# Performance work log

Measured on AMD Instinct MI355X. Metric: run time of the kernel, lower is better.

The kernel has to match this reference:

```python
import jax, jax.numpy as jnp
import numpy as np

B, NE, NMAX = 256, 90, 270
ZE = PE = GE = PPS = 32
NPROPS = 20
FP, SGE, LATH = 256, 64, 128
PIN = FP + SGE + LATH  # 448 = pred_inp_size = conv input (add_to_node)
C1, C2, H = 448, 256, 3
P1 = P2 = 512
EPS = 1e-5

PNAMES = ['sg_emb_table','lat_W1','lat_b1','lat_bn1_g','lat_bn1_b','lat_bn1_m','lat_bn1_v',
          'lat_W2','lat_b2','lat_bn2_g','lat_bn2_b','lat_bn2_m','lat_bn2_v',
          'z_emb_table','period_table','group_table','props','W_props','b_props','W_phys','b_phys',
          'gat1_W','gat1_as','gat1_ad','gat1_b','gat2_W','gat2_as','gat2_ad','gat2_b',
          'pW1','pb1','pbn1_g','pbn1_b','pbn1_m','pbn1_v',
          'pW2','pb2','pbn2_g','pbn2_b','pbn2_m','pbn2_v','pW3','pb3']

def _bn(x, g, b, m, v):
    return (x - m) * g / jnp.sqrt(v + EPS) + b

def _lrelu(x, s=0.2):
    return jnp.where(x >= 0, x, s * x)

def _gat(x, adj, W, a_s, a_d, bias):
    # PyG DenseGATConv: concat=False (mean over heads), dropout=0, negative_slope=0.2
    Bn, N, _ = x.shape
    h = (x @ W).reshape(Bn, N, H, -1)                      # [B,N,H,C]
    asrc = (h * a_s).sum(-1)                               # [B,N,H]
    adst = (h * a_d).sum(-1)
    alpha = asrc[:, None, :, :] + adst[:, :, None, :]      # [B,i,j,H]
    alpha = _lrelu(alpha, 0.2)
    adj_sl = jnp.maximum(adj, jnp.eye(N, dtype=adj.dtype))  # add self loops
    alpha = jnp.where(adj_sl[..., None] > 0, alpha, -jnp.inf)
    alpha = jax.nn.softmax(alpha, axis=2)                  # softmax over sources j
    out = jnp.einsum('bijh,bjhc->bihc', alpha, h)
    return out.mean(2) + bias                              # [B,N,C]

def _forward(comp, sg, lat, period_idx, group_idx, p):
    sg_x = p['sg_emb_table'][sg[:, 0]]                     # [B,SGE]
    # lattice MLP: (Linear -> BN -> LeakyReLU(True)==identity) x2
    h = _bn(lat @ p['lat_W1'] + p['lat_b1'], p['lat_bn1_g'], p['lat_bn1_b'], p['lat_bn1_m'], p['lat_bn1_v'])
    lat_x = _bn(h @ p['lat_W2'] + p['lat_b2'], p['lat_bn2_g'], p['lat_bn2_b'], p['lat_bn2_m'], p['lat_bn2_v'])
    # ragged -> dense batch: expand composition counts into dense node-type grid
    n_atoms = comp.sum(1)                                  # [B]
    cum = jnp.cumsum(comp, axis=1)                         # [B,NE]
    t = jnp.arange(NMAX)
    z = jax.vmap(lambda c: jnp.searchsorted(c, t, side='right'))(cum)  # [B,NMAX]
    mask = t[None, :] < n_atoms[:, None]                   # [B,NMAX] valid nodes
    z = jnp.where(mask, z, 0)
    # PhysEmbedding: z/period/group embeddings + projected properties -> final proj
    phys = jnp.concatenate([
        p['z_emb_table'][z],
        p['period_table'][period_idx[z]],
        p['group_table'][group_idx[z]],
        p['props'][z] @ p['W_props'] + p['b_props'],
    ], axis=-1)
    phys = phys @ p['W_phys'] + p['b_phys']                # [B,NMAX,FP]
    # add_to_node: cat graph-level lat/sg embeddings onto every node, then zero-pad
    node = jnp.concatenate([
        phys,
        jnp.broadcast_to(lat_x[:, None, :], (lat_x.shape[0], NMAX, LATH)),
        jnp.broadcast_to(sg_x[:, None, :], (sg_x.shape[0], NMAX, SGE)),
    ], axis=-1)
    node = node * mask[..., None].astype(node.dtype)       # to_dense_batch zero padding
    # per-graph dense block adjacency, zero diagonal (fill_diagonal_(0))
    adj = (mask[:, :, None] & mask[:, None, :]).astype(node.dtype)
    adj = adj * (1.0 - jnp.eye(NMAX, dtype=node.dtype))
    # GNNBlock: act = LeakyReLU(True) == identity (negative_slope=1)
    x1 = _gat(node, adj, p['gat1_W'], p['gat1_as'], p['gat1_ad'], p['gat1_b'])
    x2 = _gat(x1, adj, p['gat2_W'], p['gat2_as'], p['gat2_ad'], p['gat2_b'])
    comp_x = x2.sum(1)                                     # sum over ALL NMAX slots (incl. padding, as torch does)
    feat = jnp.concatenate([comp_x, sg_x, lat_x], axis=-1) # [B,PIN]
    # prediction head (eval: dropout off, BN running stats)
    h = _lrelu(_bn(feat @ p['pW1'] + p['pb1'], p['pbn1_g'], p['pbn1_b'], p['pbn1_m'], p['pbn1_v']))
    h = _lrelu(_bn(h @ p['pW2'] + p['pb2'], p['pbn2_g'], p['pbn2_b'], p['pbn2_m'], p['pbn2_v']))
    return h @ p['pW3'] + p['pb3']                         # [B,1]

def setup_inputs():
    key = jax.random.key(0)
    ks = iter(jax.random.split(key, 64))
    def nrm(shape, s=0.05):
        return jax.random.normal(next(ks), shape, dtype=jnp.float32) * s
    comp = jax.random.randint(next(ks), (B, NE), 0, 4, dtype=jnp.int32)
    comp = comp.at[0].set(3)  # graph 0 has exactly NMAX atoms -> data N_max == NMAX
    sg = jax.random.randint(next(ks), (B, 1), 0, 230)
    lat = jax.random.uniform(next(ks), (B, 6), dtype=jnp.float32)
    period_idx = jax.random.randint(next(ks), (NE,), 0, 8)
    group_idx = jax.random.randint(next(ks), (NE,), 0, 19)
    inp = dict(comp=comp, sg=sg, lat=lat, period_idx=period_idx, group_idx=group_idx)
    inp.update(
        sg_emb_table=nrm((230, SGE)),
        lat_W1=nrm((6, LATH)), lat_b1=nrm((LATH,)),
        lat_bn1_g=jnp.ones(LATH), lat_bn1_b=jnp.zeros(LATH), lat_bn1_m=jnp.zeros(LATH), lat_bn1_v=jnp.ones(LATH),
        lat_W2=nrm((LATH, LATH)), lat_b2=nrm((LATH,)),
        lat_bn2_g=jnp.ones(LATH), lat_bn2_b=jnp.zeros(LATH), lat_bn2_m=jnp.zeros(LATH), lat_bn2_v=jnp.ones(LATH),
        z_emb_table=nrm((NE, ZE)), period_table=nrm((8, PE)), group_table=nrm((19, GE)),
        props=nrm((NE, NPROPS), 0.1), W_props=nrm((NPROPS, PPS)), b_props=nrm((PPS,)),
        W_phys=nrm((ZE + PE + GE + PPS, FP)), b_phys=nrm((FP,)),
        gat1_W=nrm((PIN, H * C1)), gat1_as=nrm((H, C1)), gat1_ad=nrm((H, C1)), gat1_b=nrm((C1,)),
        gat2_W=nrm((C1, H * C2)), gat2_as=nrm((H, C2)), gat2_ad=nrm((H, C2)), gat2_b=nrm((C2,)),
        pW1=nrm((PIN, P1)), pb1=nrm((P1,)),
        pbn1_g=jnp.ones(P1), pbn1_b=jnp.zeros(P1), pbn1_m=jnp.zeros(P1), pbn1_v=jnp.ones(P1),
        pW2=nrm((P1, P2)), pb2=nrm((P2,)),
        pbn2_g=jnp.ones(P2), pbn2_b=jnp.zeros(P2), pbn2_m=jnp.zeros(P2), pbn2_v=jnp.ones(P2),
        pW3=nrm((P2, 1)), pb3=nrm((1,)),
    )
    return inp

def reference(comp, sg, lat, period_idx, group_idx,
              sg_emb_table, lat_W1, lat_b1, lat_bn1_g, lat_bn1_b, lat_bn1_m, lat_bn1_v,
              lat_W2, lat_b2, lat_bn2_g, lat_bn2_b, lat_bn2_m, lat_bn2_v,
              z_emb_table, period_table, group_table, props, W_props, b_props, W_phys, b_phys,
              gat1_W, gat1_as, gat1_ad, gat1_b, gat2_W, gat2_as, gat2_ad, gat2_b,
              pW1, pb1, pbn1_g, pbn1_b, pbn1_m, pbn1_v,
              pW2, pb2, pbn2_g, pbn2_b, pbn2_m, pbn2_v, pW3, pb3):
    vals = (sg_emb_table, lat_W1, lat_b1, lat_bn1_g, lat_bn1_b, lat_bn1_m, lat_bn1_v,
            lat_W2, lat_b2, lat_bn2_g, lat_bn2_b, lat_bn2_m, lat_bn2_v,
            z_emb_table, period_table, group_table, props, W_props, b_props, W_phys, b_phys,
            gat1_W, gat1_as, gat1_ad, gat1_b, gat2_W, gat2_as, gat2_ad, gat2_b,
            pW1, pb1, pbn1_g, pbn1_b, pbn1_m, pbn1_v,
            pW2, pb2, pbn2_g, pbn2_b, pbn2_m, pbn2_v, pW3, pb3)
    p = dict(zip(PNAMES, vals))
    return _forward(comp, sg, lat, period_idx, group_idx, p)
```

## Files before the change

### kernel.cpp

```cpp
#include <hip/hip_runtime.h>
#include <math.h>

#define BB 256
#define NEL 90
#define NMAX 270
#define C1 448
#define C2 256
#define PIN 448
#define LATH 128
#define SGE 64
#define P1 512
#define EPSB 1e-5f

typedef short shortx8 __attribute__((ext_vector_type(8)));
typedef float floatx4 __attribute__((ext_vector_type(4)));

__device__ __forceinline__ float bf2f(unsigned short u) {
  return __uint_as_float(((unsigned)u) << 16);
}
__device__ __forceinline__ unsigned short f2bf(float f) {
  unsigned x = __float_as_uint(f);
  unsigned r = (x + 0x7fffu + ((x >> 16) & 1u)) >> 16;
  return (unsigned short)r;
}
__device__ __forceinline__ void gld16(const void* g, void* l) {
  __builtin_amdgcn_global_load_lds(
      (const __attribute__((address_space(1))) unsigned int*)g,
      (__attribute__((address_space(3))) unsigned int*)l, 16, 0, 0);
}

#define NB_PREP  BB
#define NB_SCAN  1
#define NB_PHYS  NEL
#define NB_WP1   (14 * 42)
#define NB_WP2   (14 * 24)
#define NB_FOLD  112
#define NB_PAD   64
#define SETUP_GRID (NB_PREP + NB_SCAN + NB_PHYS + NB_WP1 + NB_WP2 + 2 * NB_FOLD + NB_PAD)

__global__ __launch_bounds__(256) void k_setup(
    const int* __restrict__ comp, const int* __restrict__ sg, const float* __restrict__ lat,
    const float* __restrict__ sg_emb,
    const float* __restrict__ lW1, const float* __restrict__ lb1,
    const float* __restrict__ lg1, const float* __restrict__ lbe1,
    const float* __restrict__ lm1, const float* __restrict__ lv1,
    const float* __restrict__ lW2, const float* __restrict__ lb2,
    const float* __restrict__ lg2, const float* __restrict__ lbe2,
    const float* __restrict__ lm2, const float* __restrict__ lv2,
    const int* __restrict__ period_idx, const int* __restrict__ group_idx,
    const float* __restrict__ z_emb, const float* __restrict__ period_t,
    const float* __restrict__ group_t, const float* __restrict__ props,
    const float* __restrict__ Wp, const float* __restrict__ bp,
    const float* __restrict__ Wphys, const float* __restrict__ bphys,
    const float* __restrict__ gat1_W, const float* __restrict__ gat1_as,
    const float* __restrict__ gat1_ad, const float* __restrict__ gat1_b,
    const float* __restrict__ gat2_W, const float* __restrict__ gat2_as,
    const float* __restrict__ gat2_ad, const float* __restrict__ gat2_b,
    float* __restrict__ sgx, float* __restrict__ latx, int* __restrict__ z,
    int* __restrict__ natoms, int* __restrict__ off, int* __restrict__ aoff,
    float* __restrict__ zerobuf, float* __restrict__ physpe,
    unsigned short* __restrict__ wt1, unsigned short* __restrict__ wt2,
    float* __restrict__ wsv1, float* __restrict__ wdv1,
    float* __restrict__ wsv2, float* __restrict__ wdv2, float* __restrict__ pad2) {
  int r = blockIdx.x;
  int tid = threadIdx.x;
  int wv = tid >> 6, lane = tid & 63;

  if (r < NB_PREP) {
    int b = r;
    __shared__ int cum[NEL];
    __shared__ float hbuf[LATH];
    __shared__ float latl[6];
    if (tid == 0) {
      int s = 0;
      for (int e = 0; e < NEL; ++e) { s += comp[b * NEL + e]; cum[e] = s; }
    }
    if (tid < 6) latl[tid] = lat[b * 6 + tid];
    __syncthreads();
    int n = cum[NEL - 1];
    for (int t = tid; t < NMAX; t += 256) {
      int zz = -1;
      if (t < n) {
        for (int e = 0; e < NEL; ++e) { if (cum[e] > t) { zz = e; break; } }
      }
      z[b * NMAX + t] = zz;
    }
    if (tid < SGE) sgx[b * SGE + tid] = sg_emb[sg[b] * SGE + tid];
    if (tid < LATH) {
      float acc = lb1[tid];
      for (int k = 0; k < 6; ++k) acc += latl[k] * lW1[k * LATH + tid];
      acc = (acc - lm1[tid]) * lg1[tid] * rsqrtf(lv1[tid] + EPSB) + lbe1[tid];
      hbuf[tid] = acc;
    }
    __syncthreads();
    if (tid < LATH) {
      float acc = lb2[tid];
      for (int k = 0; k < LATH; ++k) acc += hbuf[k] * lW2[k * LATH + tid];
      acc = (acc - lm2[tid]) * lg2[tid] * rsqrtf(lv2[tid] + EPSB) + lbe2[tid];
      latx[b * LATH + tid] = acc;
    }
    return;
  }
  r -= NB_PREP;
  if (r < NB_SCAN) {
    __shared__ int sh[BB];
    zerobuf[tid] = 0.f;
    int v0 = 0;
    for (int e = 0; e < NEL; ++e) v0 += comp[tid * NEL + e];
    natoms[tid] = v0;
    sh[tid] = v0;
    for (int d = 1; d < BB; d <<= 1) {
      __syncthreads();
      int v = (tid >= d) ? sh[tid - d] : 0;
      __syncthreads();
      sh[tid] += v;
    }
    __syncthreads();
    off[tid] = sh[tid] - v0;
    __syncthreads();
    int sz = 3 * ((((v0 + 15) >> 4) << 4)) * ((((v0 + 31) >> 5) << 5));
    sh[tid] = sz;
    for (int d = 1; d < BB; d <<= 1) {
      __syncthreads();
      int v = (tid >= d) ? sh[tid - d] : 0;
      __syncthreads();
      sh[tid] += v;
    }
    __syncthreads();
    aoff[tid] = sh[tid] - sz;
    return;
  }
  r -= NB_SCAN;
  if (r < NB_PHYS) {
    int e = r;
    __shared__ float ph[128];
    if (tid < 32) ph[tid] = z_emb[e * 32 + tid];
    else if (tid < 64) ph[tid] = period_t[period_idx[e] * 32 + tid - 32];
    else if (tid < 96) ph[tid] = group_t[group_idx[e] * 32 + tid - 64];
    else if (tid < 128) {
      int j = tid - 96;
      float acc = bp[j];
      for (int k = 0; k < 20; ++k) acc += props[e * 20 + k] * Wp[k * 32 + j];
      ph[tid] = acc;
    }
    __syncthreads();
    float acc = bphys[tid];
    for (int k = 0; k < 128; ++k) acc += ph[k] * Wphys[k * 256 + tid];
    physpe[e * 256 + tid] = acc;
    return;
  }
  r -= NB_PHYS;
  if (r < NB_WP1 + NB_WP2) {
    const float* W;
    unsigned short* Wt;
    int NC3, bx, by;
    if (r < NB_WP1) { W = gat1_W; Wt = wt1; NC3 = 3 * C1; bx = r % 14; by = r / 14; }
    else { int r2 = r - NB_WP1; W = gat2_W; Wt = wt2; NC3 = 3 * C2; bx = r2 % 14; by = r2 / 14; }
    int k0 = bx << 5, c0 = by << 5;
    __shared__ float ts[32][33];
    int e4 = tid << 2;
    int kk = e4 >> 5, cc = e4 & 31;
    float4 v = *(const float4*)(W + (size_t)(k0 + kk) * NC3 + c0 + cc);
    ts[kk][cc] = v.x; ts[kk][cc + 1] = v.y; ts[kk][cc + 2] = v.z; ts[kk][cc + 3] = v.w;
    __syncthreads();
    int c2 = tid & 31, kg = tid >> 5;
    ushort4 u;
    u.x = f2bf(ts[kg * 4 + 0][c2]); u.y = f2bf(ts[kg * 4 + 1][c2]);
    u.z = f2bf(ts[kg * 4 + 2][c2]); u.w = f2bf(ts[kg * 4 + 3][c2]);
    *(ushort4*)(Wt + (size_t)(c0 + c2) * 448 + k0 + (kg << 2)) = u;
    return;
  }
  r -= NB_WP1 + NB_WP2;
  if (r < 2 * NB_FOLD) {
    const float* W; const float* as_; const float* ad_;
    float* wsv; float* wdv; int NC3, C, kb;
    if (r < NB_FOLD) { W = gat1_W; as_ = gat1_as; ad_ = gat1_ad; wsv = wsv1; wdv = wdv1; NC3 = 3 * C1; C = C1; kb = r << 2; }
    else { int r2 = r - NB_FOLD; W = gat2_W; as_ = gat2_as; ad_ = gat2_ad; wsv = wsv2; wdv = wdv2; NC3 = 3 * C2; C = C2; kb = r2 << 2; }
    int k = kb + wv;
    for (int h = 0; h < 3; ++h) {
      float ss = 0.f, sd = 0.f;
      for (int c = lane; c < C; c += 64) {
        float wvv = W[(size_t)k * NC3 + h * C + c];
        ss += wvv * as_[h * C + c];
        sd += wvv * ad_[h * C + c];
      }
      for (int o = 32; o > 0; o >>= 1) { ss += __shfl_xor(ss, o); sd += __shfl_xor(sd, o); }
      if (lane == 0) { wsv[k * 3 + h] = ss; wdv[k * 3 + h] = sd; }
    }
    return;
  }
  r -= 2 * NB_FOLD;
  {
    int c = (r << 2) + wv;
    float s = 0.f;
    for (int k = lane; k < C1; k += 64) {
      const float* wr = gat2_W + (size_t)k * (3 * C2) + c;
      s += gat1_b[k] * (wr[0] + wr[C2] + wr[2 * C2]);
    }
    for (int o = 32; o > 0; o >>= 1) s += __shfl_xor(s, o);
    if (lane == 0) pad2[c] = s * (1.f / 3.f) + gat2_b[c];
  }
}

__global__ __launch_bounds__(256) void k_nodep(
    const int* __restrict__ z, const int* __restrict__ off, const int* __restrict__ natoms,
    const float* __restrict__ physpe, const float* __restrict__ latx,
    const float* __restrict__ sgx, unsigned short* __restrict__ x0) {
  int b = blockIdx.x;
  int n = natoms[b], ob = off[b];
  int tid = threadIdx.x;
  __shared__ int zl[NMAX];
  for (int t = tid; t < n; t += 256) zl[t] = z[b * NMAX + t];
  __syncthreads();
  int items = n * 56;
  for (int e = tid; e < items; e += 256) {
    int t = e / 56, c8 = (e - t * 56) << 3;
    int zt = zl[t];
    float v[8];
    if (c8 < 256) {
      float4 a = *(const float4*)(physpe + zt * 256 + c8);
      float4 c = *(const float4*)(physpe + zt * 256 + c8 + 4);
      v[0] = a.x; v[1] = a.y; v[2] = a.z; v[3] = a.w;
      v[4] = c.x; v[5] = c.y; v[6] = c.z; v[7] = c.w;
    } else if (c8 < 384) {
      float4 a = *(const float4*)(latx + b * LATH + c8 - 256);
      float4 c = *(const float4*)(latx + b * LATH + c8 - 252);
      v[0] = a.x; v[1] = a.y; v[2] = a.z; v[3] = a.w;
      v[4] = c.x; v[5] = c.y; v[6] = c.z; v[7] = c.w;
    } else {
      float4 a = *(const float4*)(sgx + b * SGE + c8 - 384);
      float4 c = *(const float4*)(sgx + b * SGE + c8 - 380);
      v[0] = a.x; v[1] = a.y; v[2] = a.z; v[3] = a.w;
      v[4] = c.x; v[5] = c.y; v[6] = c.z; v[7] = c.w;
    }
    unsigned short u[8];
    #pragma unroll
    for (int i = 0; i < 8; ++i) u[i] = f2bf(v[i]);
    *(uint4*)(x0 + (size_t)(ob + t) * PIN + c8) = *(uint4*)u;
  }
}

__global__ __launch_bounds__(256) void k_av2(
    const unsigned short* __restrict__ x, const float* __restrict__ wsv,
    const float* __restrict__ wdv, const int* __restrict__ off,
    const int* __restrict__ natoms, float* __restrict__ asrc,
    float* __restrict__ adst, int K) {
  __shared__ float sw[C1 * 3], dw[C1 * 3];
  int tid = threadIdx.x;
  for (int e = tid; e < K * 3; e += 256) { sw[e] = wsv[e]; dw[e] = wdv[e]; }
  __syncthreads();
  int total = off[BB - 1] + natoms[BB - 1];
  int wv = tid >> 6, lane = tid & 63;
  int nk8 = K >> 3;
  int stride = gridDim.x << 2;
  for (int row = (blockIdx.x << 2) + wv; row < total; row += stride) {
    float s0 = 0.f, s1 = 0.f, s2 = 0.f, d0 = 0.f, d1 = 0.f, d2 = 0.f;
    if (lane < nk8) {
      uint4 raw = *(const uint4*)(x + (size_t)row * K + (lane << 3));
      unsigned short us[8];
      *(uint4*)us = raw;
      #pragma unroll
      for (int u = 0; u < 8; ++u) {
        float xv = bf2f(us[u]);
        int kb = ((lane << 3) + u) * 3;
        s0 += xv * sw[kb + 0]; s1 += xv * sw[kb + 1]; s2 += xv * sw[kb + 2];
        d0 += xv * dw[kb + 0]; d1 += xv * dw[kb + 1]; d2 += xv * dw[kb + 2];
      }
    }
    #pragma unroll
    for (int o = 32; o > 0; o >>= 1) {
      s0 += __shfl_xor(s0, o); s1 += __shfl_xor(s1, o); s2 += __shfl_xor(s2, o);
      d0 += __shfl_xor(d0, o); d1 += __shfl_xor(d1, o); d2 += __shfl_xor(d2, o);
    }
    if (lane == 0) {
      asrc[row * 3 + 0] = s0; asrc[row * 3 + 1] = s1; asrc[row * 3 + 2] = s2;
      adst[row * 3 + 0] = d0; adst[row * 3 + 1] = d1; adst[row * 3 + 2] = d2;
    }
  }
}

#define MTMAX 17
__global__ __launch_bounds__(256) void k_alpha(
    const float* __restrict__ asrc, const float* __restrict__ adst,
    const int* __restrict__ off, const int* __restrict__ natoms,
    const int* __restrict__ aoff, unsigned short* __restrict__ alpha) {
  int bid = blockIdx.x;
  int b = bid & (BB - 1);
  int hm = bid >> 8;
  int h = hm % 3;
  int mt = hm / 3;
  int n = natoms[b];
  if (n == 0) return;
  int mtn = (n + 15) >> 4;
  if (mt >= mtn) return;
  int ktn = (n + 31) >> 5;
  int rext = mtn << 4, kext = ktn << 5;
  int ob = off[b];
  size_t ab = (size_t)aoff[b] + (size_t)h * rext * kext;
  int tid = threadIdx.x;
  int wv = tid >> 6, lane = tid & 63;
  __shared__ float asl[288];
  for (int j = tid; j < kext; j += 256)
    asl[j] = (j < n) ? asrc[(ob + j) * 3 + h] : 0.f;
  __syncthreads();
  #pragma unroll
  for (int r = 0; r < 4; ++r) {
    int i = (mt << 4) + (wv << 2) + r;
    unsigned short* rowp = alpha + ab + (size_t)i * kext;
    if (i >= n) {
      for (int j = lane; j < kext; j += 64) rowp[j] = 0;
      continue;
    }
    float ad = adst[(ob + i) * 3 + h];
    float m = -1e30f;
    for (int j = lane; j < n; j += 64) {
      float sc = asl[j] + ad;
      sc = fmaxf(sc, 0.2f * sc);
      m = fmaxf(m, sc);
    }
    for (int o = 32; o > 0; o >>= 1) m = fmaxf(m, __shfl_xor(m, o));
    float s = 0.f;
    for (int j = lane; j < n; j += 64) {
      float sc = asl[j] + ad;
      sc = fmaxf(sc, 0.2f * sc);
      s += __expf(sc - m);
    }
    for (int o = 32; o > 0; o >>= 1) s += __shfl_xor(s, o);
    float rs = 1.f / s;
    for (int j = lane; j < kext; j += 64) {
      float v = 0.f;
      if (j < n) {
        float sc = asl[j] + ad;
        sc = fmaxf(sc, 0.2f * sc);
        v = __expf(sc - m) * rs;
      }
      rowp[j] = f2bf(v);
    }
  }
}

#define MTW 5

__global__ __launch_bounds__(256, 2) void k_fused_mfma(
    const unsigned short* __restrict__ xin, const unsigned short* __restrict__ Wt,
    const unsigned short* __restrict__ alpha, const int* __restrict__ aoff,
    const int* __restrict__ off, const int* __restrict__ natoms,
    const float* __restrict__ bias, const float* __restrict__ zerobuf,
    unsigned short* __restrict__ xout, int K, int C, int NC) {
  int bid = blockIdx.x;
  int xg = bid & 7;
  int g = bid >> 3;
  int cblk = g % NC;
  int b = xg + ((g / NC) << 3);
  int c0 = cblk << 6;
  int n = natoms[b];
  if (n == 0) return;
  int ob = off[b];
  size_t ab = (size_t)aoff[b];
  int tid = threadIdx.x;
  int wv = tid >> 6;
  int lane = tid & 63;
  int m16 = lane & 15;
  int q = lane >> 4;

  int mtn = (n + 15) >> 4;
  int jmax = mtn << 4;
  int ktn = (n + 31) >> 5;
  int kext = ktn << 5;
  size_t hstride = (size_t)jmax * kext;

  __shared__ unsigned short xs0[17 * 512];
  __shared__ unsigned short tt[36 * 512];

  const unsigned short* xsrc[MTW];
  #pragma unroll
  for (int t_i = 0; t_i < MTW; ++t_i) {
    int mt = wv + (t_i << 2);
    int j = (mt << 4) + m16;
    xsrc[t_i] = (j < n) ? (xin + (size_t)(ob + j) * K + (q << 3))
                        : (const unsigned short*)zerobuf;
  }

  floatx4 acc[MTW][4];
  #pragma unroll
  for (int i = 0; i < MTW; ++i)
    #pragma unroll
    for (int nt = 0; nt < 4; ++nt) acc[i][nt] = (floatx4)0.f;

  for (int h = 0; h < 3; ++h) {
    floatx4 tac[MTW][4];
    #pragma unroll
    for (int i = 0; i < MTW; ++i)
      #pragma unroll
      for (int nt = 0; nt < 4; ++nt) tac[i][nt] = (floatx4)0.f;

    const unsigned short* wsrc = Wt + (size_t)(h * C + c0 + lane) * K + (wv << 3);

    #pragma unroll
    for (int t_i = 0; t_i < MTW; ++t_i) {
      int mt = wv + (t_i << 2);
      if (mt < mtn) gld16(xsrc[t_i], &xs0[mt << 9]);
    }
    gld16(wsrc, &tt[wv << 9]);
    __syncthreads();

    int buf = 0;
    for (int k0 = 0; k0 < K; k0 += 32) {
      int k1 = k0 + 32;
      if (k1 < K) {
        unsigned short* xnext = (buf == 0) ? (tt + 4096) : xs0;
        #pragma unroll
        for (int t_i = 0; t_i < MTW; ++t_i) {
          int mt = wv + (t_i << 2);
          if (mt < mtn) gld16(xsrc[t_i] + k1, xnext + (mt << 9));
        }
        gld16(wsrc + k1, &tt[((buf ^ 1) << 11) + (wv << 9)]);
      }
      const unsigned short* wb = &tt[buf << 11];
      const unsigned short* xb = (buf == 0) ? xs0 : (tt + 4096);
      shortx8 bfr[4];
      #pragma unroll
      for (int nt = 0; nt < 4; ++nt)
        bfr[nt] = *(const shortx8*)(wb + (q << 9) + (((nt << 4) + m16) << 3));
      #pragma unroll
      for (int t_i = 0; t_i < MTW; ++t_i) {
        int mt = wv + (t_i << 2);
        if (mt < mtn) {
          shortx8 a = *(const shortx8*)(xb + (mt << 9) + (((q << 4) + m16) << 3));
          #pragma unroll
          for (int nt = 0; nt < 4; ++nt)
            tac[t_i][nt] = __builtin_amdgcn_mfma_f32_16x16x32_bf16(a, bfr[nt], tac[t_i][nt], 0, 0, 0);
        }
      }
      __syncthreads();
      buf ^= 1;
    }
    #pragma unroll
    for (int t_i = 0; t_i < MTW; ++t_i) {
      int mt = wv + (t_i << 2);
      if (mt < mtn) {
        int jbase = (mt << 4) + (q << 2);
        #pragma unroll
        for (int nt = 0; nt < 4; ++nt) {
          floatx4 d = tac[t_i][nt];
          ushort4 u;
          u.x = f2bf(d.x); u.y = f2bf(d.y); u.z = f2bf(d.z); u.w = f2bf(d.w);
          int c = (nt << 4) + m16;
          *(ushort4*)(tt + ((jbase >> 3) << 9) + (c << 3) + (jbase & 7)) = u;
        }
      }
    }
    for (int e = tid; e < ((kext - jmax) << 6); e += 256) {
      int j = jmax + (e >> 6), c = e & 63;
      tt[((j >> 3) << 9) + (c << 3) + (j & 7)] = 0;
    }
    __syncthreads();
    const unsigned short* ap = alpha + ab + (size_t)h * hstride;
    for (int k0p = 0; k0p < kext; k0p += 32) {
      shortx8 tb[4];
      #pragma unroll
      for (int nt = 0; nt < 4; ++nt)
        tb[nt] = *(const shortx8*)(tt + (((k0p >> 3) + q) << 9) + (((nt << 4) + m16) << 3));
      #pragma unroll
      for (int t_i = 0; t_i < MTW; ++t_i) {
        int mt = wv + (t_i << 2);
        if (mt < mtn) {
          shortx8 af = *(const shortx8*)(ap + (size_t)((mt << 4) + m16) * kext + k0p + (q << 3));
          #pragma unroll
          for (int nt = 0; nt < 4; ++nt)
            acc[t_i][nt] = __builtin_amdgcn_mfma_f32_16x16x32_bf16(af, tb[nt], acc[t_i][nt], 0, 0, 0);
        }
      }
    }
    __syncthreads();
  }
  float bq[4];
  #pragma unroll
  for (int nt = 0; nt < 4; ++nt) bq[nt] = bias[c0 + (nt << 4) + m16];
  const float inv3 = 1.f / 3.f;
  #pragma unroll
  for (int t_i = 0; t_i < MTW; ++t_i) {
    int mt = wv + (t_i << 2);
    if (mt < mtn) {
      #pragma unroll
      for (int nt = 0; nt < 4; ++nt) {
        floatx4 d = acc[t_i][nt];
        int cidx = c0 + (nt << 4) + m16;
        #pragma unroll
        for (int r = 0; r < 4; ++r) {
          int i = (mt << 4) + (q << 2) + r;
          if (i < n) xout[(size_t)(ob + i) * C + cidx] = f2bf(d[r] * inv3 + bq[nt]);
        }
      }
    }
  }
}

__global__ __launch_bounds__(512) void k_feat_head(
    const unsigned short* __restrict__ x2, const float* __restrict__ pad2,
    const int* __restrict__ off, const int* __restrict__ natoms,
    const float* __restrict__ sgx, const float* __restrict__ latx,
    const float* __restrict__ W1, const float* __restrict__ b1,
    const float* __restrict__ g1, const float* __restrict__ be1,
    const float* __restrict__ m1, const float* __restrict__ v1,
    const float* __restrict__ W2, const float* __restrict__ b2,
    const float* __restrict__ g2, const float* __restrict__ be2,
    const float* __restrict__ m2, const float* __restrict__ v2,
    const float* __restrict__ W3, const float* __restrict__ b3,
    float* __restrict__ out) {
  int b = blockIdx.x, tid = threadIdx.x;
  int wv8 = tid >> 6, lane = tid & 63;
  int n = natoms[b], ob = off[b];
  __shared__ float part[8][256];
  __shared__ float f[PIN];
  __shared__ float h1[P1];
  __shared__ float h2[P1];
  __shared__ float red[512];
  float a0 = 0.f, a1 = 0.f, a2 = 0.f, a3 = 0.f;
  for (int r = wv8; r < n; r += 8) {
    uint2 raw = *(const uint2*)(x2 + (size_t)(ob + r) * C2 + (lane << 2));
    unsigned short us[4];
    *(uint2*)us = raw;
    a0 += bf2f(us[0]); a1 += bf2f(us[1]); a2 += bf2f(us[2]); a3 += bf2f(us[3]);
  }
  {
    float4 p = make_float4(a0, a1, a2, a3);
    *(float4*)&part[wv8][lane << 2] = p;
  }
  __syncthreads();
  if (tid < 256) {
    float s = 0.f;
    #pragma unroll
    for (int w = 0; w < 8; ++w) s += part[w][tid];
    f[tid] = s + (float)(NMAX - n) * pad2[tid];
  } else if (tid < 320) {
    f[tid] = sgx[b * SGE + (tid - 256)];
  } else if (tid < 448) {
    f[tid] = latx[b * LATH + (tid - 320)];
  }
  __syncthreads();
  {
    int o = tid;
    float acc = b1[o];
    for (int k = 0; k < PIN; ++k) acc += f[k] * W1[k * P1 + o];
    acc = (acc - m1[o]) * g1[o] * rsqrtf(v1[o] + EPSB) + be1[o];
    h1[o] = acc >= 0.f ? acc : 0.2f * acc;
  }
  __syncthreads();
  {
    int o = tid;
    float acc = b2[o];
    for (int k = 0; k < P1; ++k) acc += h1[k] * W2[k * P1 + o];
    acc = (acc - m2[o]) * g2[o] * rsqrtf(v2[o] + EPSB) + be2[o];
    h2[o] = acc >= 0.f ? acc : 0.2f * acc;
  }
  __syncthreads();
  red[tid] = h2[tid] * W3[tid];
  __syncthreads();
  for (int s = 256; s > 0; s >>= 1) {
    if (tid < s) red[tid] += red[tid + s];
    __syncthreads();
  }
  if (tid == 0) out[b] = red[0] + b3[0];
}

extern "C" void kernel_launch(void* const* d_in, const int* in_sizes, int n_in,
                              void* d_out, int out_size, void* d_ws, size_t ws_size,
                              hipStream_t stream) {
  const int*   comp       = (const int*)d_in[0];
  const int*   sg         = (const int*)d_in[1];
  const float* lat        = (const float*)d_in[2];
  const int*   period_idx = (const int*)d_in[3];
  const int*   group_idx  = (const int*)d_in[4];
  const float* sg_emb     = (const float*)d_in[5];
  const float* lat_W1     = (const float*)d_in[6];
  const float* lat_b1     = (const float*)d_in[7];
  const float* lat_bn1_g  = (const float*)d_in[8];
  const float* lat_bn1_b  = (const float*)d_in[9];
  const float* lat_bn1_m  = (const float*)d_in[10];
  const float* lat_bn1_v  = (const float*)d_in[11];
  const float* lat_W2     = (const float*)d_in[12];
  const float* lat_b2     = (const float*)d_in[13];
  const float* lat_bn2_g  = (const float*)d_in[14];
  const float* lat_bn2_b  = (const float*)d_in[15];
  const float* lat_bn2_m  = (const float*)d_in[16];
  const float* lat_bn2_v  = (const float*)d_in[17];
  const float* z_emb      = (const float*)d_in[18];
  const float* period_t   = (const float*)d_in[19];
  const float* group_t    = (const float*)d_in[20];
  const float* props      = (const float*)d_in[21];
  const float* W_props    = (const float*)d_in[22];
  const float* b_props    = (const float*)d_in[23];
  const float* W_phys     = (const float*)d_in[24];
  const float* b_phys     = (const float*)d_in[25];
  const float* gat1_W     = (const float*)d_in[26];
  const float* gat1_as    = (const float*)d_in[27];
  const float* gat1_ad    = (const float*)d_in[28];
  const float* gat1_b     = (const float*)d_in[29];
  const float* gat2_W     = (const float*)d_in[30];
  const float* gat2_as    = (const float*)d_in[31];
  const float* gat2_ad    = (const float*)d_in[32];
  const float* gat2_b     = (const float*)d_in[33];
  const float* pW1        = (const float*)d_in[34];
  const float* pb1        = (const float*)d_in[35];
  const float* pbn1_g     = (const float*)d_in[36];
  const float* pbn1_b     = (const float*)d_in[37];
  const float* pbn1_m     = (const float*)d_in[38];
  const float* pbn1_v     = (const float*)d_in[39];
  const float* pW2        = (const float*)d_in[40];
  const float* pb2        = (const float*)d_in[41];
  const float* pbn2_g     = (const float*)d_in[42];
  const float* pbn2_b     = (const float*)d_in[43];
  const float* pbn2_m     = (const float*)d_in[44];
  const float* pbn2_v     = (const float*)d_in[45];
  const float* pW3        = (const float*)d_in[46];
  const float* pb3        = (const float*)d_in[47];

  float* ws = (float*)d_ws;
  const size_t o_sgx  = 0;
  const size_t o_latx = o_sgx  + (size_t)BB * SGE;
  const size_t o_nat  = o_latx + (size_t)BB * LATH;
  const size_t o_off  = o_nat  + BB;
  const size_t o_aoff = o_off  + BB;
  const size_t o_z    = o_aoff + BB;
  const size_t o_phys = o_z    + (size_t)BB * NMAX;
  const size_t o_wsv1 = o_phys + (size_t)NEL * 256;
  const size_t o_wdv1 = o_wsv1 + (size_t)C1 * 3;
  const size_t o_wsv2 = o_wdv1 + (size_t)C1 * 3;
  const size_t o_wdv2 = o_wsv2 + (size_t)C1 * 3;
  const size_t o_asrc = o_wdv2 + (size_t)C1 * 3;
  const size_t o_adst = o_asrc + (size_t)BB * NMAX * 3;
  const size_t o_pad2 = o_adst + (size_t)BB * NMAX * 3;
  const size_t o_zero = o_pad2 + 256;
  const size_t o_wt1  = o_zero + 256;
  const size_t o_wt2  = o_wt1  + (size_t)(3 * C1) * PIN / 2;
  const size_t o_x0   = o_wt2  + (size_t)(3 * C2) * C1 / 2;
  const size_t o_x1   = o_x0   + (size_t)BB * NMAX * PIN / 2;
  const size_t o_alph = o_x1   + (size_t)BB * NMAX * PIN / 2;

  float* sgx    = ws + o_sgx;
  float* latx   = ws + o_latx;
  int*   natoms = (int*)(ws + o_nat);
  int*   off    = (int*)(ws + o_off);
  int*   aoff   = (int*)(ws + o_aoff);
  int*   z      = (int*)(ws + o_z);
  float* physpe = ws + o_phys;
  float* wsv1   = ws + o_wsv1;
  float* wdv1   = ws + o_wdv1;
  float* wsv2   = ws + o_wsv2;
  float* wdv2   = ws + o_wdv2;
  float* asrc   = ws + o_asrc;
  float* adst   = ws + o_adst;
  float* pad2   = ws + o_pad2;
  float* zerobuf = ws + o_zero;
  unsigned short* wt1   = (unsigned short*)(ws + o_wt1);
  unsigned short* wt2   = (unsigned short*)(ws + o_wt2);
  unsigned short* x0    = (unsigned short*)(ws + o_x0);
  unsigned short* x1    = (unsigned short*)(ws + o_x1);
  unsigned short* x2    = x0;
  unsigned short* alpha = (unsigned short*)(ws + o_alph);

  const int ALG = BB * 3 * MTMAX;

  k_setup<<<SETUP_GRID, 256, 0, stream>>>(
      comp, sg, lat, sg_emb,
      lat_W1, lat_b1, lat_bn1_g, lat_bn1_b, lat_bn1_m, lat_bn1_v,
      lat_W2, lat_b2, lat_bn2_g, lat_bn2_b, lat_bn2_m, lat_bn2_v,
      period_idx, group_idx, z_emb, period_t, group_t, props,
      W_props, b_props, W_phys, b_phys,
      gat1_W, gat1_as, gat1_ad, gat1_b,
      gat2_W, gat2_as, gat2_ad, gat2_b,
      sgx, latx, z, natoms, off, aoff, zerobuf, physpe,
      wt1, wt2, wsv1, wdv1, wsv2, wdv2, pad2);

  k_nodep<<<BB, 256, 0, stream>>>(z, off, natoms, physpe, latx, sgx, x0);

  k_av2<<<1024, 256, 0, stream>>>(x0, wsv1, wdv1, off, natoms, asrc, adst, PIN);
  k_alpha<<<ALG, 256, 0, stream>>>(asrc, adst, off, natoms, aoff, alpha);
  k_fused_mfma<<<(C1 / 64) * BB, 256, 0, stream>>>(x0, wt1, alpha, aoff,
      off, natoms, gat1_b, zerobuf, x1, PIN, C1, C1 / 64);

  k_av2<<<1024, 256, 0, stream>>>(x1, wsv2, wdv2, off, natoms, asrc, adst, C1);
  k_alpha<<<ALG, 256, 0, stream>>>(asrc, adst, off, natoms, aoff, alpha);
  k_fused_mfma<<<(C2 / 64) * BB, 256, 0, stream>>>(x1, wt2, alpha, aoff,
      off, natoms, gat2_b, zerobuf, x2, C1, C2, C2 / 64);

  k_feat_head<<<BB, 512, 0, stream>>>(x2, pad2, off, natoms, sgx, latx,
      pW1, pb1, pbn1_g, pbn1_b, pbn1_m, pbn1_v,
      pW2, pb2, pbn2_g, pbn2_b, pbn2_m, pbn2_v,
      pW3, pb3, (float*)d_out);
}
```

Measured before the change: 741.7 us.

## Triple-buffer GAT MFMA K-loop with vmcnt-counted async loads

Replaces the two-buffer K loop in the fused GAT MFMA kernel with a three-stage LDS ring in dynamic shared memory (64 KB). Global-to-LDS loads run two k-steps ahead, and each step waits with a vmcnt threshold followed by one barrier, instead of a full sync at the end of every step. Wave-inactive tiles issue dummy loads into a scratch slot so every thread has the same outstanding-load count. The loop is fully unrolled for a hardcoded 14 k-steps, which ties the kernel to K=448, and the larger LDS footprint may limit how many blocks fit per CU.

New measurement: 1.036 ms. 1.4x slower.

```diff
diff --git a/kernel.cpp b/kernel.cpp
--- a/kernel.cpp
+++ b/kernel.cpp
@@ -340,6 +340,8 @@
 }
 
 #define MTW 5
+#define STG_X 8704
+#define STG_SZ 10752
 
 __global__ __launch_bounds__(256, 2) void k_fused_mfma(
     const unsigned short* __restrict__ xin, const unsigned short* __restrict__ Wt,
@@ -347,6 +349,7 @@
     const int* __restrict__ off, const int* __restrict__ natoms,
     const float* __restrict__ bias, const float* __restrict__ zerobuf,
     unsigned short* __restrict__ xout, int K, int C, int NC) {
+  extern __shared__ unsigned short smem[];
   int bid = blockIdx.x;
   int xg = bid & 7;
   int g = bid >> 3;
@@ -369,8 +372,12 @@
   int kext = ktn << 5;
   size_t hstride = (size_t)jmax * kext;
 
-  __shared__ unsigned short xs0[17 * 512];
-  __shared__ unsigned short tt[36 * 512];
+  unsigned short* st0 = smem;
+  unsigned short* st1 = smem + STG_SZ;
+  unsigned short* st2 = smem + 2 * STG_SZ;
+  unsigned short* dump = smem + 3 * STG_SZ;
+  unsigned short* tt = smem;
+  unsigned short* bufs[3] = {st0, st1, st2};
 
   const unsigned short* xsrc[MTW];
   #pragma unroll
@@ -396,28 +403,18 @@
 
     const unsigned short* wsrc = Wt + (size_t)(h * C + c0 + lane) * K + (wv << 3);
 
-    #pragma unroll
-    for (int t_i = 0; t_i < MTW; ++t_i) {
-      int mt = wv + (t_i << 2);
-      if (mt < mtn) gld16(xsrc[t_i], &xs0[mt << 9]);
-    }
-    gld16(wsrc, &tt[wv << 9]);
-    __syncthreads();
-
-    int buf = 0;
-    for (int k0 = 0; k0 < K; k0 += 32) {
-      int k1 = k0 + 32;
-      if (k1 < K) {
-        unsigned short* xnext = (buf == 0) ? (tt + 4096) : xs0;
-        #pragma unroll
-        for (int t_i = 0; t_i < MTW; ++t_i) {
-          int mt = wv + (t_i << 2);
-          if (mt < mtn) gld16(xsrc[t_i] + k1, xnext + (mt << 9));
-        }
-        gld16(wsrc + k1, &tt[((buf ^ 1) << 11) + (wv << 9)]);
-      }
-      const unsigned short* wb = &tt[buf << 11];
-      const unsigned short* xb = (buf == 0) ? xs0 : (tt + 4096);
+    auto issue = [&](int kstep, unsigned short* stg) {
+      int k1 = kstep << 5;
+      #pragma unroll
+      for (int t_i = 0; t_i < MTW; ++t_i) {
+        int mt = wv + (t_i << 2);
+        if (mt < mtn) gld16(xsrc[t_i] + k1, stg + (mt << 9));
+        else gld16(zerobuf, dump);
+      }
+      gld16(wsrc + k1, stg + STG_X + (wv << 9));
+    };
+    auto consume = [&](const unsigned short* stg) {
+      const unsigned short* wb = stg + STG_X;
       shortx8 bfr[4];
       #pragma unroll
       for (int nt = 0; nt < 4; ++nt)
@@ -426,15 +423,30 @@
       for (int t_i = 0; t_i < MTW; ++t_i) {
         int mt = wv + (t_i << 2);
         if (mt < mtn) {
-          shortx8 a = *(const shortx8*)(xb + (mt << 9) + (((q << 4) + m16) << 3));
+          shortx8 a = *(const shortx8*)(stg + (mt << 9) + (((q << 4) + m16) << 3));
           #pragma unroll
           for (int nt = 0; nt < 4; ++nt)
             tac[t_i][nt] = __builtin_amdgcn_mfma_f32_16x16x32_bf16(a, bfr[nt], tac[t_i][nt], 0, 0, 0);
         }
       }
-      __syncthreads();
-      buf ^= 1;
-    }
+    };
+
+    issue(0, st0);
+    issue(1, st1);
+    #pragma unroll
+    for (int s = 0; s < 13; ++s) {
+      asm volatile("s_waitcnt vmcnt(6)" ::: "memory");
+      __builtin_amdgcn_s_barrier();
+      __builtin_amdgcn_sched_barrier(0);
+      if (s < 12) issue(s + 2, bufs[(s + 2) % 3]);
+      consume(bufs[s % 3]);
+    }
+    asm volatile("s_waitcnt vmcnt(0)" ::: "memory");
+    __builtin_amdgcn_s_barrier();
+    __builtin_amdgcn_sched_barrier(0);
+    consume(st1);
+    __syncthreads();
+
     #pragma unroll
     for (int t_i = 0; t_i < MTW; ++t_i) {
       int mt = wv + (t_i << 2);
@@ -677,12 +689,12 @@
 
   k_av2<<<1024, 256, 0, stream>>>(x0, wsv1, wdv1, off, natoms, asrc, adst, PIN);
   k_alpha<<<ALG, 256, 0, stream>>>(asrc, adst, off, natoms, aoff, alpha);
-  k_fused_mfma<<<(C1 / 64) * BB, 256, 0, stream>>>(x0, wt1, alpha, aoff,
+  k_fused_mfma<<<(C1 / 64) * BB, 256, 65536, stream>>>(x0, wt1, alpha, aoff,
       off, natoms, gat1_b, zerobuf, x1, PIN, C1, C1 / 64);
 
   k_av2<<<1024, 256, 0, stream>>>(x1, wsv2, wdv2, off, natoms, asrc, adst, C1);
   k_alpha<<<ALG, 256, 0, stream>>>(asrc, adst, off, natoms, aoff, alpha);
-  k_fused_mfma<<<(C2 / 64) * BB, 256, 0, stream>>>(x1, wt2, alpha, aoff,
+  k_fused_mfma<<<(C2 / 64) * BB, 256, 65536, stream>>>(x1, wt2, alpha, aoff,
       off, natoms, gat2_b, zerobuf, x2, C1, C2, C2 / 64);
 
   k_feat_head<<<BB, 512, 0, stream>>>(x2, pad2, off, natoms, sgx, latx,
```
